# Kernel tuning notes

Measured on AMD Instinct MI355X. Metric: run time of the kernel, lower is better.

The kernel has to match this reference:

```python
import jax, jax.numpy as jnp
import numpy as np

N, C, NS = 131072, 128, 16
BN_EPS = 1e-5


def setup_inputs() -> dict:
    key = jax.random.key(0)
    ks = jax.random.split(key, 8)
    p = jax.random.normal(ks[0], (N, 3), dtype=jnp.float32)
    u = jax.random.normal(ks[1], (N, C), dtype=jnp.float32)
    o = jnp.array([N], dtype=jnp.int32)  # batch offset (single cloud)
    idx = jax.random.randint(ks[2], (N, NS), 0, N, dtype=jnp.int32)  # precomputed KNN indices
    s = 1.0 / np.sqrt(C)
    W1 = jax.random.uniform(ks[3], (C, C), jnp.float32, -s, s)
    b1 = jax.random.uniform(ks[4], (C,), jnp.float32, -s, s)
    W2 = jax.random.uniform(ks[5], (C, C), jnp.float32, -s, s)
    b2 = jax.random.uniform(ks[6], (C,), jnp.float32, -s, s)
    gamma = jnp.ones((C,), jnp.float32)
    beta = jnp.zeros((C,), jnp.float32)
    return {"p": p, "u": u, "o": o, "idx": idx, "W1": W1, "b1": b1,
            "W2": W2, "b2": b2, "gamma": gamma, "beta": beta}


def reference(p, u, o, idx, W1, b1, W2, b2, gamma, beta):
    # pre_trans: Linear(d_in, d_in)
    u_pre = u @ W1 + b1                                  # [N, C]
    # queryandgroup (use_xyz=False): gather neighbor features by KNN idx
    u_n = u_pre[idx]                                     # [N, NS, C] irregular gather
    # local Laplacian: ReLU(neighbor - center), mean over neighborhood
    lap = jnp.maximum(u_n - u_pre[:, None, :], 0.0).mean(axis=1)  # [N, C]
    # varphi: Linear -> BatchNorm1d (training stats) -> ReLU
    h = lap @ W2 + b2                                    # [N, C]
    mean = h.mean(axis=0)
    var = ((h - mean) ** 2).mean(axis=0)  # biased var, as BN normalization uses
    h = (h - mean) * jax.lax.rsqrt(var + BN_EPS) * gamma + beta
    u_tt = jnp.maximum(h, 0.0)
    return (p, u_tt, o)
```

## Files before the change

### kernel.cpp

```cpp
#include <hip/hip_runtime.h>

#define N_PTS 131072
#define C_DIM 128
#define NS_K  16
#define BN_EPS 1e-5f

typedef unsigned short ushort_t;
typedef unsigned short u16x8 __attribute__((ext_vector_type(8)));
typedef __bf16 bf16x8 __attribute__((ext_vector_type(8)));
typedef float f32x4 __attribute__((ext_vector_type(4)));

__device__ __forceinline__ ushort_t f2b(float f) {
    unsigned int u = __float_as_uint(f);
    u += 0x7FFFu + ((u >> 16) & 1u);
    return (ushort_t)(u >> 16);
}
__device__ __forceinline__ float b2f(ushort_t h) {
    return __uint_as_float((unsigned int)h << 16);
}

__global__ __launch_bounds__(256) void prep_w_kernel(
    const float* __restrict__ W1, const float* __restrict__ W2,
    ushort_t* __restrict__ wT1, ushort_t* __restrict__ wT2)
{
    const int t = blockIdx.x * 256 + threadIdx.x;
    const int n = t & 127;
    const int k = t >> 7;
    wT1[n * 128 + k] = f2b(W1[k * 128 + n]);
    wT2[n * 128 + k] = f2b(W2[k * 128 + n]);
}

template <bool A_BF16, bool STATS>
__global__ __launch_bounds__(256) void gemm_mfma_kernel(
    const void* __restrict__ Aptr, const ushort_t* __restrict__ wT,
    const float* __restrict__ bias, ushort_t* __restrict__ out,
    float* __restrict__ gsum, float* __restrict__ gsq)
{
    __shared__ __align__(16) ushort_t a_sh[128 * 136];
    __shared__ __align__(16) ushort_t w_sh[128 * 136];
    __shared__ float s_sum[128];
    __shared__ float s_sq[128];

    const int tid  = threadIdx.x;
    const int lane = tid & 63;
    const int wv   = tid >> 6;
    const int m16  = lane & 15;
    const int q    = lane >> 4;
    const int base = blockIdx.x * 128;

    if (STATS && tid < 128) { s_sum[tid] = 0.f; s_sq[tid] = 0.f; }

    {
        const int row  = tid >> 1;
        const int half = (tid & 1) * 64;
        ushort_t* as = a_sh + row * 136 + half;
        if (A_BF16) {
            const ushort_t* ag = (const ushort_t*)Aptr + (size_t)(base + row) * 128 + half;
            #pragma unroll
            for (int j = 0; j < 8; j++)
                *(u16x8*)(as + j * 8) = *(const u16x8*)(ag + j * 8);
        } else {
            const float* ag = (const float*)Aptr + (size_t)(base + row) * 128 + half;
            #pragma unroll
            for (int j = 0; j < 8; j++) {
                f32x4 lo = *(const f32x4*)(ag + j * 8);
                f32x4 hi = *(const f32x4*)(ag + j * 8 + 4);
                u16x8 v;
                v[0] = f2b(lo[0]); v[1] = f2b(lo[1]); v[2] = f2b(lo[2]); v[3] = f2b(lo[3]);
                v[4] = f2b(hi[0]); v[5] = f2b(hi[1]); v[6] = f2b(hi[2]); v[7] = f2b(hi[3]);
                *(u16x8*)(as + j * 8) = v;
            }
        }
    }
    {
        const int n    = tid >> 1;
        const int half = (tid & 1) * 64;
        const ushort_t* wg = wT + (size_t)n * 128 + half;
        ushort_t* ws = w_sh + n * 136 + half;
        #pragma unroll
        for (int j = 0; j < 8; j++)
            *(u16x8*)(ws + j * 8) = *(const u16x8*)(wg + j * 8);
    }
    __syncthreads();

    f32x4 acc[2][8];
    #pragma unroll
    for (int i = 0; i < 2; i++)
        #pragma unroll
        for (int c = 0; c < 8; c++) acc[i][c] = (f32x4){0.f, 0.f, 0.f, 0.f};

    const ushort_t* ap0 = a_sh + ((wv * 2 + 0) * 16 + m16) * 136 + q * 8;
    const ushort_t* ap1 = a_sh + ((wv * 2 + 1) * 16 + m16) * 136 + q * 8;
    const ushort_t* wp  = w_sh + m16 * 136 + q * 8;

    #pragma unroll
    for (int k0 = 0; k0 < 128; k0 += 32) {
        bf16x8 a0 = __builtin_bit_cast(bf16x8, *(const u16x8*)(ap0 + k0));
        bf16x8 a1 = __builtin_bit_cast(bf16x8, *(const u16x8*)(ap1 + k0));
        #pragma unroll
        for (int c = 0; c < 8; c++) {
            bf16x8 b = __builtin_bit_cast(bf16x8, *(const u16x8*)(wp + c * (16 * 136) + k0));
            acc[0][c] = __builtin_amdgcn_mfma_f32_16x16x32_bf16(a0, b, acc[0][c], 0, 0, 0);
            acc[1][c] = __builtin_amdgcn_mfma_f32_16x16x32_bf16(a1, b, acc[1][c], 0, 0, 0);
        }
    }

    __syncthreads();

    float psum[8], psq[8];
    #pragma unroll
    for (int c = 0; c < 8; c++) { psum[c] = 0.f; psq[c] = 0.f; }

    #pragma unroll
    for (int c = 0; c < 8; c++) {
        const int col = c * 16 + m16;
        const float bv = bias[col];
        #pragma unroll
        for (int i = 0; i < 2; i++) {
            const int rb = (wv * 2 + i) * 16 + q * 4;
            #pragma unroll
            for (int r = 0; r < 4; r++) {
                const float v = acc[i][c][r] + bv;
                a_sh[(rb + r) * 136 + col] = f2b(v);
                if (STATS) { psum[c] += v; psq[c] += v * v; }
            }
        }
    }
    if (STATS) {
        #pragma unroll
        for (int c = 0; c < 8; c++) {
            atomicAdd(&s_sum[c * 16 + m16], psum[c]);
            atomicAdd(&s_sq[c * 16 + m16],  psq[c]);
        }
    }
    __syncthreads();

    {
        const int r0 = tid >> 4;
        const int c0 = (tid & 15) * 8;
        #pragma unroll
        for (int it = 0; it < 8; it++) {
            const int rl = r0 + it * 16;
            const u16x8 v = *(const u16x8*)(a_sh + rl * 136 + c0);
            *(u16x8*)(out + (size_t)(base + rl) * 128 + c0) = v;
        }
    }
    if (STATS && tid < 128) {
        atomicAdd(&gsum[tid], s_sum[tid]);
        atomicAdd(&gsq[tid],  s_sq[tid]);
    }
}

__global__ __launch_bounds__(256) void lap_gemm_kernel(
    const ushort_t* __restrict__ table, const int* __restrict__ idx,
    const ushort_t* __restrict__ wT, const float* __restrict__ bias,
    ushort_t* __restrict__ out, float* __restrict__ gsum, float* __restrict__ gsq)
{
    __shared__ __align__(16) ushort_t a_sh[128 * 136];
    __shared__ __align__(16) ushort_t w_sh[128 * 136];
    __shared__ __align__(16) int s_idx[128 * NS_K];
    __shared__ float s_sum[128];
    __shared__ float s_sq[128];

    const int tid  = threadIdx.x;
    const int lane = tid & 63;
    const int wv   = tid >> 6;
    const int m16  = lane & 15;
    const int q    = lane >> 4;
    const int base = blockIdx.x * 128;

    if (tid < 128) { s_sum[tid] = 0.f; s_sq[tid] = 0.f; }

    {
        const int4* ig = (const int4*)(idx + (size_t)base * NS_K);
        int4* is = (int4*)s_idx;
        is[tid]       = ig[tid];
        is[tid + 256] = ig[tid + 256];
    }
    {
        const int n    = tid >> 1;
        const int half = (tid & 1) * 64;
        const ushort_t* wg = wT + (size_t)n * 128 + half;
        ushort_t* ws = w_sh + n * 136 + half;
        #pragma unroll
        for (int j = 0; j < 8; j++)
            *(u16x8*)(ws + j * 8) = *(const u16x8*)(wg + j * 8);
    }
    __syncthreads();

    {
        const int pl = tid >> 4;
        const int c8 = (tid & 15) * 8;
        #pragma unroll 1
        for (int it = 0; it < 8; it++) {
            const int pp = it * 16 + pl;
            const u16x8 cv = *(const u16x8*)(table + (size_t)(base + pp) * 128 + c8);
            float ctr[8];
            #pragma unroll
            for (int e = 0; e < 8; e++) ctr[e] = b2f(cv[e]);

            float lacc[8];
            #pragma unroll
            for (int e = 0; e < 8; e++) lacc[e] = 0.f;

            #pragma unroll
            for (int s = 0; s < NS_K; s++) {
                const int j = s_idx[pp * NS_K + s];
                const u16x8 nv = *(const u16x8*)(table + (size_t)j * 128 + c8);
                #pragma unroll
                for (int e = 0; e < 8; e++)
                    lacc[e] += fmaxf(b2f(nv[e]) - ctr[e], 0.f);
            }
            u16x8 ov;
            #pragma unroll
            for (int e = 0; e < 8; e++) ov[e] = f2b(lacc[e] * (1.f / (float)NS_K));
            *(u16x8*)(a_sh + pp * 136 + c8) = ov;
        }
    }
    __syncthreads();

    f32x4 acc[2][8];
    #pragma unroll
    for (int i = 0; i < 2; i++)
        #pragma unroll
        for (int c = 0; c < 8; c++) acc[i][c] = (f32x4){0.f, 0.f, 0.f, 0.f};

    const ushort_t* ap0 = a_sh + ((wv * 2 + 0) * 16 + m16) * 136 + q * 8;
    const ushort_t* ap1 = a_sh + ((wv * 2 + 1) * 16 + m16) * 136 + q * 8;
    const ushort_t* wp  = w_sh + m16 * 136 + q * 8;

    #pragma unroll
    for (int k0 = 0; k0 < 128; k0 += 32) {
        bf16x8 a0 = __builtin_bit_cast(bf16x8, *(const u16x8*)(ap0 + k0));
        bf16x8 a1 = __builtin_bit_cast(bf16x8, *(const u16x8*)(ap1 + k0));
        #pragma unroll
        for (int c = 0; c < 8; c++) {
            bf16x8 b = __builtin_bit_cast(bf16x8, *(const u16x8*)(wp + c * (16 * 136) + k0));
            acc[0][c] = __builtin_amdgcn_mfma_f32_16x16x32_bf16(a0, b, acc[0][c], 0, 0, 0);
            acc[1][c] = __builtin_amdgcn_mfma_f32_16x16x32_bf16(a1, b, acc[1][c], 0, 0, 0);
        }
    }

    __syncthreads();

    float psum[8], psq[8];
    #pragma unroll
    for (int c = 0; c < 8; c++) { psum[c] = 0.f; psq[c] = 0.f; }

    #pragma unroll
    for (int c = 0; c < 8; c++) {
        const int col = c * 16 + m16;
        const float bv = bias[col];
        #pragma unroll
        for (int i = 0; i < 2; i++) {
            const int rb = (wv * 2 + i) * 16 + q * 4;
            #pragma unroll
            for (int r = 0; r < 4; r++) {
                const float v = acc[i][c][r] + bv;
                a_sh[(rb + r) * 136 + col] = f2b(v);
                psum[c] += v; psq[c] += v * v;
            }
        }
    }
    #pragma unroll
    for (int c = 0; c < 8; c++) {
        atomicAdd(&s_sum[c * 16 + m16], psum[c]);
        atomicAdd(&s_sq[c * 16 + m16],  psq[c]);
    }
    __syncthreads();

    {
        const int r0 = tid >> 4;
        const int c0 = (tid & 15) * 8;
        #pragma unroll
        for (int it = 0; it < 8; it++) {
            const int rl = r0 + it * 16;
            const u16x8 v = *(const u16x8*)(a_sh + rl * 136 + c0);
            *(u16x8*)(out + (size_t)(base + rl) * 128 + c0) = v;
        }
    }
    if (tid < 128) {
        atomicAdd(&gsum[tid], s_sum[tid]);
        atomicAdd(&gsq[tid],  s_sq[tid]);
    }
}

__global__ void bn_stats_kernel(const float* __restrict__ gsum,
                                const float* __restrict__ gsq,
                                const float* __restrict__ gamma,
                                const float* __restrict__ beta,
                                float* __restrict__ bnsc, float* __restrict__ bnsh)
{
    const int c = threadIdx.x;
    const float invN = 1.f / (float)N_PTS;
    const float mean = gsum[c] * invN;
    const float var  = gsq[c] * invN - mean * mean;
    const float sc   = rsqrtf(var + BN_EPS) * gamma[c];
    bnsc[c] = sc;
    bnsh[c] = fmaf(-mean, sc, beta[c]);
}

#define BN_BLOCKS ((N_PTS * C_DIM / 8) / 256)
#define P_BLOCKS  ((3 * N_PTS / 4) / 256)

__global__ __launch_bounds__(256) void bn_relu_p_kernel(
    const ushort_t* __restrict__ h, const float* __restrict__ bnsc,
    const float* __restrict__ bnsh, const float* __restrict__ p,
    const int* __restrict__ o, float* __restrict__ out)
{
    const int b = blockIdx.x;
    if (b < BN_BLOCKS) {
        const size_t i = (size_t)b * 256 + threadIdx.x;
        const int c8 = (threadIdx.x * 8) & 127;

        const u16x8 hv = *(const u16x8*)(h + i * 8);
        const f32x4 sc0 = *(const f32x4*)(bnsc + c8);
        const f32x4 sc1 = *(const f32x4*)(bnsc + c8 + 4);
        const f32x4 sh0 = *(const f32x4*)(bnsh + c8);
        const f32x4 sh1 = *(const f32x4*)(bnsh + c8 + 4);

        f32x4 o0, o1;
        #pragma unroll
        for (int e = 0; e < 4; e++) {
            o0[e] = fmaxf(fmaf(b2f(hv[e]),     sc0[e], sh0[e]), 0.f);
            o1[e] = fmaxf(fmaf(b2f(hv[4 + e]), sc1[e], sh1[e]), 0.f);
        }
        float* op = out + (size_t)3 * N_PTS + i * 8;
        *(f32x4*)(op)     = o0;
        *(f32x4*)(op + 4) = o1;
    } else {
        const size_t i = (size_t)(b - BN_BLOCKS) * 256 + threadIdx.x;
        *(f32x4*)(out + i * 4) = *(const f32x4*)(p + i * 4);
        if (i == 0)
            out[(size_t)3 * N_PTS + (size_t)N_PTS * C_DIM] = (float)o[0];
    }
}

extern "C" void kernel_launch(void* const* d_in, const int* in_sizes, int n_in,
                              void* d_out, int out_size, void* d_ws, size_t ws_size,
                              hipStream_t stream) {
    const float* p     = (const float*)d_in[0];
    const float* u     = (const float*)d_in[1];
    const int*   o     = (const int*)d_in[2];
    const int*   idx   = (const int*)d_in[3];
    const float* W1    = (const float*)d_in[4];
    const float* b1    = (const float*)d_in[5];
    const float* W2    = (const float*)d_in[6];
    const float* b2    = (const float*)d_in[7];
    const float* gamma = (const float*)d_in[8];
    const float* beta  = (const float*)d_in[9];
    float* out = (float*)d_out;

    char* ws = (char*)d_ws;
    const size_t buf_bytes = (size_t)N_PTS * C_DIM * sizeof(ushort_t);
    ushort_t* table = (ushort_t*)ws;
    ushort_t* h     = (ushort_t*)(ws + buf_bytes);
    float*    stats = (float*)(ws + 2 * buf_bytes);
    float* gsum = stats;
    float* gsq  = stats + 128;
    float* bnsc = stats + 256;
    float* bnsh = stats + 384;
    ushort_t* wT1 = (ushort_t*)(stats + 512);
    ushort_t* wT2 = wT1 + 128 * 128;

    hipMemsetAsync(stats, 0, 256 * sizeof(float), stream);

    prep_w_kernel<<<64, 256, 0, stream>>>(W1, W2, wT1, wT2);
    gemm_mfma_kernel<false, false><<<N_PTS / 128, 256, 0, stream>>>(
        u, wT1, b1, table, nullptr, nullptr);
    lap_gemm_kernel<<<N_PTS / 128, 256, 0, stream>>>(
        table, idx, wT2, b2, h, gsum, gsq);
    bn_stats_kernel<<<1, 128, 0, stream>>>(gsum, gsq, gamma, beta, bnsc, bnsh);
    bn_relu_p_kernel<<<BN_BLOCKS + P_BLOCKS, 256, 0, stream>>>(
        h, bnsc, bnsh, p, o, out);
}
```

Baseline: 286.6 us.

## Drop shared weight and index staging to raise occupancy in GEMM kernels

Removes the LDS copies of the transposed weight matrix and the KNN index tile. Weight fragments are now read straight from global memory (L1/L2-cached) inside the MFMA loop, and neighbour indices are loaded per point as int4 vectors into registers. Together with launch_bounds(256,4), this cuts LDS use per block so more blocks can be resident, giving more latency hiding for the irregular gather. The trade-off is repeated global or cache reads of the weights during the MFMA loop and higher register pressure from the 16 indices held per point.

```diff
diff --git a/kernel.cpp b/kernel.cpp
--- a/kernel.cpp
+++ b/kernel.cpp
@@ -31,13 +31,12 @@
 }
 
 template <bool A_BF16, bool STATS>
-__global__ __launch_bounds__(256) void gemm_mfma_kernel(
+__global__ __launch_bounds__(256, 4) void gemm_mfma_kernel(
     const void* __restrict__ Aptr, const ushort_t* __restrict__ wT,
     const float* __restrict__ bias, ushort_t* __restrict__ out,
     float* __restrict__ gsum, float* __restrict__ gsq)
 {
     __shared__ __align__(16) ushort_t a_sh[128 * 136];
-    __shared__ __align__(16) ushort_t w_sh[128 * 136];
     __shared__ float s_sum[128];
     __shared__ float s_sq[128];
 
@@ -72,15 +71,6 @@
             }
         }
     }
-    {
-        const int n    = tid >> 1;
-        const int half = (tid & 1) * 64;
-        const ushort_t* wg = wT + (size_t)n * 128 + half;
-        ushort_t* ws = w_sh + n * 136 + half;
-        #pragma unroll
-        for (int j = 0; j < 8; j++)
-            *(u16x8*)(ws + j * 8) = *(const u16x8*)(wg + j * 8);
-    }
     __syncthreads();
 
     f32x4 acc[2][8];
@@ -91,7 +81,7 @@
 
     const ushort_t* ap0 = a_sh + ((wv * 2 + 0) * 16 + m16) * 136 + q * 8;
     const ushort_t* ap1 = a_sh + ((wv * 2 + 1) * 16 + m16) * 136 + q * 8;
-    const ushort_t* wp  = w_sh + m16 * 136 + q * 8;
+    const ushort_t* wp  = wT + (size_t)m16 * 128 + q * 8;
 
     #pragma unroll
     for (int k0 = 0; k0 < 128; k0 += 32) {
@@ -99,7 +89,7 @@
         bf16x8 a1 = __builtin_bit_cast(bf16x8, *(const u16x8*)(ap1 + k0));
         #pragma unroll
         for (int c = 0; c < 8; c++) {
-            bf16x8 b = __builtin_bit_cast(bf16x8, *(const u16x8*)(wp + c * (16 * 136) + k0));
+            bf16x8 b = __builtin_bit_cast(bf16x8, *(const u16x8*)(wp + c * (16 * 128) + k0));
             acc[0][c] = __builtin_amdgcn_mfma_f32_16x16x32_bf16(a0, b, acc[0][c], 0, 0, 0);
             acc[1][c] = __builtin_amdgcn_mfma_f32_16x16x32_bf16(a1, b, acc[1][c], 0, 0, 0);
         }
@@ -151,14 +141,12 @@
     }
 }
 
-__global__ __launch_bounds__(256) void lap_gemm_kernel(
+__global__ __launch_bounds__(256, 4) void lap_gemm_kernel(
     const ushort_t* __restrict__ table, const int* __restrict__ idx,
     const ushort_t* __restrict__ wT, const float* __restrict__ bias,
     ushort_t* __restrict__ out, float* __restrict__ gsum, float* __restrict__ gsq)
 {
     __shared__ __align__(16) ushort_t a_sh[128 * 136];
-    __shared__ __align__(16) ushort_t w_sh[128 * 136];
-    __shared__ __align__(16) int s_idx[128 * NS_K];
     __shared__ float s_sum[128];
     __shared__ float s_sq[128];
 
@@ -172,29 +160,19 @@
     if (tid < 128) { s_sum[tid] = 0.f; s_sq[tid] = 0.f; }
 
     {
-        const int4* ig = (const int4*)(idx + (size_t)base * NS_K);
-        int4* is = (int4*)s_idx;
-        is[tid]       = ig[tid];
-        is[tid + 256] = ig[tid + 256];
-    }
-    {
-        const int n    = tid >> 1;
-        const int half = (tid & 1) * 64;
-        const ushort_t* wg = wT + (size_t)n * 128 + half;
-        ushort_t* ws = w_sh + n * 136 + half;
-        #pragma unroll
-        for (int j = 0; j < 8; j++)
-            *(u16x8*)(ws + j * 8) = *(const u16x8*)(wg + j * 8);
-    }
-    __syncthreads();
-
-    {
         const int pl = tid >> 4;
         const int c8 = (tid & 15) * 8;
         #pragma unroll 1
         for (int it = 0; it < 8; it++) {
             const int pp = it * 16 + pl;
-            const u16x8 cv = *(const u16x8*)(table + (size_t)(base + pp) * 128 + c8);
+            const size_t prow = (size_t)(base + pp);
+
+            const int4* ig = (const int4*)(idx + prow * NS_K);
+            const int4 i0 = ig[0], i1 = ig[1], i2 = ig[2], i3 = ig[3];
+            const int jj[16] = {i0.x, i0.y, i0.z, i0.w, i1.x, i1.y, i1.z, i1.w,
+                                i2.x, i2.y, i2.z, i2.w, i3.x, i3.y, i3.z, i3.w};
+
+            const u16x8 cv = *(const u16x8*)(table + prow * 128 + c8);
             float ctr[8];
             #pragma unroll
             for (int e = 0; e < 8; e++) ctr[e] = b2f(cv[e]);
@@ -205,8 +183,7 @@
 
             #pragma unroll
             for (int s = 0; s < NS_K; s++) {
-                const int j = s_idx[pp * NS_K + s];
-                const u16x8 nv = *(const u16x8*)(table + (size_t)j * 128 + c8);
+                const u16x8 nv = *(const u16x8*)(table + (size_t)jj[s] * 128 + c8);
                 #pragma unroll
                 for (int e = 0; e < 8; e++)
                     lacc[e] += fmaxf(b2f(nv[e]) - ctr[e], 0.f);
@@ -227,7 +204,7 @@
 
     const ushort_t* ap0 = a_sh + ((wv * 2 + 0) * 16 + m16) * 136 + q * 8;
     const ushort_t* ap1 = a_sh + ((wv * 2 + 1) * 16 + m16) * 136 + q * 8;
-    const ushort_t* wp  = w_sh + m16 * 136 + q * 8;
+    const ushort_t* wp  = wT + (size_t)m16 * 128 + q * 8;
 
     #pragma unroll
     for (int k0 = 0; k0 < 128; k0 += 32) {
@@ -235,7 +212,7 @@
         bf16x8 a1 = __builtin_bit_cast(bf16x8, *(const u16x8*)(ap1 + k0));
         #pragma unroll
         for (int c = 0; c < 8; c++) {
-            bf16x8 b = __builtin_bit_cast(bf16x8, *(const u16x8*)(wp + c * (16 * 136) + k0));
+            bf16x8 b = __builtin_bit_cast(bf16x8, *(const u16x8*)(wp + c * (16 * 128) + k0));
             acc[0][c] = __builtin_amdgcn_mfma_f32_16x16x32_bf16(a0, b, acc[0][c], 0, 0, 0);
             acc[1][c] = __builtin_amdgcn_mfma_f32_16x16x32_bf16(a1, b, acc[1][c], 0, 0, 0);
         }
```

Measured after the change: 336.1 us. 17.3% more time.
